# Kernel optimization log

Measured on AMD Instinct MI355X. Metric: run time of the kernel, lower is better.

Reference implementation:

```python
import jax, jax.numpy as jnp
import numpy as np

DEPTH = 10
N_FEATURES = 1024
N_INTERNAL = 2 ** DEPTH - 1  # 1023
N_LEAVES = 2 ** DEPTH        # 1024
BATCH = 16384


def setup_inputs() -> dict:
    key = jax.random.key(0)
    k_x, k_w, k_b, k_leaf = jax.random.split(key, 4)
    x = jax.random.normal(k_x, (BATCH, N_FEATURES), dtype=jnp.float32)
    # stacked nn.Linear(n_features, 1) weights for all internal nodes
    bound = 1.0 / np.sqrt(N_FEATURES)
    W = jax.random.uniform(k_w, (N_INTERNAL, N_FEATURES), dtype=jnp.float32, minval=-bound, maxval=bound)
    b = jax.random.uniform(k_b, (N_INTERNAL,), dtype=jnp.float32, minval=-bound, maxval=bound)
    leaf_values = jax.random.normal(k_leaf, (N_LEAVES, 1), dtype=jnp.float32) * 0.01
    return {"x": x, "W": W, "b": b, "leaf_values": leaf_values}


def reference(x, W, b, leaf_values):
    # all node gates in one GEMM: [B, n_internal]
    gates = jax.nn.sigmoid(x @ W.T + b)
    # leaf path bits, MSB-first (matches path[::-1] in the original).
    # NOTE: original code increments node_index 0..depth-1 for every leaf
    # (it does NOT do binary-tree child indexing) -- replicated faithfully.
    leaf_ids = jnp.arange(N_LEAVES)
    shifts = DEPTH - 1 - jnp.arange(DEPTH)
    bits = ((leaf_ids[:, None] >> shifts[None, :]) & 1).astype(bool)  # [L, D]
    prob = jnp.ones((x.shape[0], N_LEAVES), dtype=x.dtype)  # [B, L]
    for d in range(DEPTH):  # small fixed loop over tree depth
        p = gates[:, d:d + 1]  # [B, 1]
        prob = prob * jnp.where(bits[:, d][None, :], p, 1.0 - p)
    return prob @ leaf_values  # [B, 1]
```

## Files before the change

### kernel.cpp

```cpp
#include <hip/hip_runtime.h>

#define BATCH      16384
#define NF         1024
#define TREE_DEPTH 10

__global__ __launch_bounds__(256, 2)
void sdt_kernel(const float* __restrict__ x,
                const float* __restrict__ W,
                const float* __restrict__ b,
                const float* __restrict__ leaf,
                float* __restrict__ out,
                int nwaves_total)
{
    const int lane = threadIdx.x & 63;
    const int wid  = (int)((blockIdx.x * blockDim.x + threadIdx.x) >> 6);

    float4 Wr[10][4];
#pragma unroll
    for (int d = 0; d < 10; ++d)
#pragma unroll
        for (int k = 0; k < 4; ++k)
            Wr[d][k] = *reinterpret_cast<const float4*>(W + d * NF + k * 256 + 4 * lane);

    float bias[10];
#pragma unroll
    for (int d = 0; d < 10; ++d) bias[d] = b[d];

    float Lv[16];
#pragma unroll
    for (int k = 0; k < 4; ++k) {
        float4 t = *reinterpret_cast<const float4*>(leaf + 16 * lane + 4 * k);
        Lv[4 * k + 0] = t.x; Lv[4 * k + 1] = t.y;
        Lv[4 * k + 2] = t.z; Lv[4 * k + 3] = t.w;
    }

    float4 xv[4];
    {
        const float* xr = x + (size_t)wid * NF;
#pragma unroll
        for (int k = 0; k < 4; ++k)
            xv[k] = *reinterpret_cast<const float4*>(xr + k * 256 + 4 * lane);
    }

    for (int row = wid; row < BATCH; row += nwaves_total) {
        float4 xn[4];
        const int nrow = row + nwaves_total;
        if (nrow < BATCH) {
            const float* xr = x + (size_t)nrow * NF;
#pragma unroll
            for (int k = 0; k < 4; ++k)
                xn[k] = *reinterpret_cast<const float4*>(xr + k * 256 + 4 * lane);
        }

        float acc[10];
#pragma unroll
        for (int d = 0; d < 10; ++d) {
            float a = 0.0f;
#pragma unroll
            for (int k = 0; k < 4; ++k) {
                a = fmaf(xv[k].x, Wr[d][k].x, a);
                a = fmaf(xv[k].y, Wr[d][k].y, a);
                a = fmaf(xv[k].z, Wr[d][k].z, a);
                a = fmaf(xv[k].w, Wr[d][k].w, a);
            }
            acc[d] = a;
        }

#pragma unroll
        for (int d = 0; d < 10; ++d) {
            float a = acc[d];
#pragma unroll
            for (int off = 32; off > 0; off >>= 1)
                a += __shfl_xor(a, off, 64);
            acc[d] = a;
        }

        float g[10];
#pragma unroll
        for (int d = 0; d < 10; ++d) {
            float z = acc[d] + bias[d];
            g[d] = __builtin_amdgcn_rcpf(1.0f + __expf(-z));
        }

        float s9[8];
#pragma unroll
        for (int j = 0; j < 8; ++j)
            s9[j] = fmaf(g[9], Lv[2 * j + 1] - Lv[2 * j], Lv[2 * j]);
        float s8[4];
#pragma unroll
        for (int j = 0; j < 4; ++j)
            s8[j] = fmaf(g[8], s9[2 * j + 1] - s9[2 * j], s9[2 * j]);
        float s7[2];
#pragma unroll
        for (int j = 0; j < 2; ++j)
            s7[j] = fmaf(g[7], s8[2 * j + 1] - s8[2 * j], s8[2 * j]);
        float s6 = fmaf(g[6], s7[1] - s7[0], s7[0]);

        float w = 1.0f;
#pragma unroll
        for (int d = 0; d < 6; ++d) {
            int bit = (lane >> (5 - d)) & 1;
            w *= bit ? g[d] : (1.0f - g[d]);
        }

        float v = w * s6;
#pragma unroll
        for (int off = 32; off > 0; off >>= 1)
            v += __shfl_xor(v, off, 64);

        if (lane == 0) out[row] = v;

#pragma unroll
        for (int k = 0; k < 4; ++k) xv[k] = xn[k];
    }
}

extern "C" void kernel_launch(void* const* d_in, const int* in_sizes, int n_in,
                              void* d_out, int out_size, void* d_ws, size_t ws_size,
                              hipStream_t stream) {
    const float* x    = (const float*)d_in[0];
    const float* W    = (const float*)d_in[1];
    const float* b    = (const float*)d_in[2];
    const float* leaf = (const float*)d_in[3];
    float* out = (float*)d_out;

    const int blocks  = 512;
    const int threads = 256;
    const int nwaves  = blocks * threads / 64;

    sdt_kernel<<<blocks, threads, 0, stream>>>(x, W, b, leaf, out, nwaves);
}
```

Before: 26.25 us.

## Process two rows per wave iteration and move leaf values to LDS

Each wave now handles a pair of adjacent rows per loop iteration and prefetches the next pair, so twice as much x data is in flight. Leaf values are staged in shared memory and reloaded each iteration instead of staying resident in registers, which frees registers for the larger prefetch buffers. The larger working set raises register pressure and may hurt occupancy under the launch bounds. Batch and wave counts are now hard-coded constants.

```diff
diff --git a/kernel.cpp b/kernel.cpp
--- a/kernel.cpp
+++ b/kernel.cpp
@@ -1,19 +1,23 @@
 #include <hip/hip_runtime.h>
 
-#define BATCH      16384
-#define NF         1024
-#define TREE_DEPTH 10
+#define BATCH   16384
+#define NF      1024
+#define NWAVES  2048
+#define NPAIRS  (BATCH / 2 / NWAVES)
 
 __global__ __launch_bounds__(256, 2)
 void sdt_kernel(const float* __restrict__ x,
                 const float* __restrict__ W,
                 const float* __restrict__ b,
                 const float* __restrict__ leaf,
-                float* __restrict__ out,
-                int nwaves_total)
+                float* __restrict__ out)
 {
     const int lane = threadIdx.x & 63;
     const int wid  = (int)((blockIdx.x * blockDim.x + threadIdx.x) >> 6);
+
+    __shared__ float lv_s[1024];
+    *reinterpret_cast<float4*>(&lv_s[threadIdx.x * 4]) =
+        *reinterpret_cast<const float4*>(leaf + threadIdx.x * 4);
 
     float4 Wr[10][4];
 #pragma unroll
@@ -26,92 +30,131 @@
 #pragma unroll
     for (int d = 0; d < 10; ++d) bias[d] = b[d];
 
-    float Lv[16];
+    __syncthreads();
+
+    float4 xv[2][4];
+    {
+        const float* xr = x + (size_t)(2 * wid) * NF;
 #pragma unroll
-    for (int k = 0; k < 4; ++k) {
-        float4 t = *reinterpret_cast<const float4*>(leaf + 16 * lane + 4 * k);
-        Lv[4 * k + 0] = t.x; Lv[4 * k + 1] = t.y;
-        Lv[4 * k + 2] = t.z; Lv[4 * k + 3] = t.w;
+        for (int r = 0; r < 2; ++r)
+#pragma unroll
+            for (int k = 0; k < 4; ++k)
+                xv[r][k] = *reinterpret_cast<const float4*>(xr + r * NF + k * 256 + 4 * lane);
     }
 
-    float4 xv[4];
-    {
-        const float* xr = x + (size_t)wid * NF;
+    for (int i = 0; i < NPAIRS; ++i) {
+        const int rowA = 2 * (wid + i * NWAVES);
+
+        float4 xn[2][4];
+        if (i + 1 < NPAIRS) {
+            const float* xr = x + (size_t)(rowA + 2 * NWAVES) * NF;
 #pragma unroll
-        for (int k = 0; k < 4; ++k)
-            xv[k] = *reinterpret_cast<const float4*>(xr + k * 256 + 4 * lane);
-    }
-
-    for (int row = wid; row < BATCH; row += nwaves_total) {
-        float4 xn[4];
-        const int nrow = row + nwaves_total;
-        if (nrow < BATCH) {
-            const float* xr = x + (size_t)nrow * NF;
+            for (int r = 0; r < 2; ++r)
 #pragma unroll
-            for (int k = 0; k < 4; ++k)
-                xn[k] = *reinterpret_cast<const float4*>(xr + k * 256 + 4 * lane);
+                for (int k = 0; k < 4; ++k)
+                    xn[r][k] = *reinterpret_cast<const float4*>(xr + r * NF + k * 256 + 4 * lane);
         }
 
-        float acc[10];
+        float accA[10];
 #pragma unroll
         for (int d = 0; d < 10; ++d) {
             float a = 0.0f;
 #pragma unroll
             for (int k = 0; k < 4; ++k) {
-                a = fmaf(xv[k].x, Wr[d][k].x, a);
-                a = fmaf(xv[k].y, Wr[d][k].y, a);
-                a = fmaf(xv[k].z, Wr[d][k].z, a);
-                a = fmaf(xv[k].w, Wr[d][k].w, a);
+                a = fmaf(xv[0][k].x, Wr[d][k].x, a);
+                a = fmaf(xv[0][k].y, Wr[d][k].y, a);
+                a = fmaf(xv[0][k].z, Wr[d][k].z, a);
+                a = fmaf(xv[0][k].w, Wr[d][k].w, a);
             }
-            acc[d] = a;
+            accA[d] = a;
+        }
+#pragma unroll
+        for (int d = 0; d < 10; ++d) {
+            float a = accA[d];
+#pragma unroll
+            for (int off = 32; off > 0; off >>= 1)
+                a += __shfl_xor(a, off, 64);
+            accA[d] = a;
+        }
+
+        float accB[10];
+#pragma unroll
+        for (int d = 0; d < 10; ++d) {
+            float a = 0.0f;
+#pragma unroll
+            for (int k = 0; k < 4; ++k) {
+                a = fmaf(xv[1][k].x, Wr[d][k].x, a);
+                a = fmaf(xv[1][k].y, Wr[d][k].y, a);
+                a = fmaf(xv[1][k].z, Wr[d][k].z, a);
+                a = fmaf(xv[1][k].w, Wr[d][k].w, a);
+            }
+            accB[d] = a;
+        }
+#pragma unroll
+        for (int d = 0; d < 10; ++d) {
+            float a = accB[d];
+#pragma unroll
+            for (int off = 32; off > 0; off >>= 1)
+                a += __shfl_xor(a, off, 64);
+            accB[d] = a;
+        }
+
+        float g[2][10];
+#pragma unroll
+        for (int d = 0; d < 10; ++d) {
+            g[0][d] = __builtin_amdgcn_rcpf(1.0f + __expf(-(accA[d] + bias[d])));
+            g[1][d] = __builtin_amdgcn_rcpf(1.0f + __expf(-(accB[d] + bias[d])));
+        }
+
+        float Lv[16];
+#pragma unroll
+        for (int k = 0; k < 4; ++k) {
+            float4 t = *reinterpret_cast<const float4*>(&lv_s[16 * lane + 4 * k]);
+            Lv[4 * k + 0] = t.x; Lv[4 * k + 1] = t.y;
+            Lv[4 * k + 2] = t.z; Lv[4 * k + 3] = t.w;
+        }
+
+        float vout[2];
+#pragma unroll
+        for (int r = 0; r < 2; ++r) {
+            float s9[8];
+#pragma unroll
+            for (int j = 0; j < 8; ++j)
+                s9[j] = fmaf(g[r][9], Lv[2 * j + 1] - Lv[2 * j], Lv[2 * j]);
+            float s8[4];
+#pragma unroll
+            for (int j = 0; j < 4; ++j)
+                s8[j] = fmaf(g[r][8], s9[2 * j + 1] - s9[2 * j], s9[2 * j]);
+            float s7[2];
+#pragma unroll
+            for (int j = 0; j < 2; ++j)
+                s7[j] = fmaf(g[r][7], s8[2 * j + 1] - s8[2 * j], s8[2 * j]);
+            float s6 = fmaf(g[r][6], s7[1] - s7[0], s7[0]);
+
+            float w = 1.0f;
+#pragma unroll
+            for (int d = 0; d < 6; ++d) {
+                int bit = (lane >> (5 - d)) & 1;
+                w *= bit ? g[r][d] : (1.0f - g[r][d]);
+            }
+
+            float v = w * s6;
+#pragma unroll
+            for (int off = 32; off > 0; off >>= 1)
+                v += __shfl_xor(v, off, 64);
+            vout[r] = v;
+        }
+
+        if (lane == 0) {
+            out[rowA]     = vout[0];
+            out[rowA + 1] = vout[1];
         }
 
 #pragma unroll
-        for (int d = 0; d < 10; ++d) {
-            float a = acc[d];
+        for (int r = 0; r < 2; ++r)
 #pragma unroll
-            for (int off = 32; off > 0; off >>= 1)
-                a += __shfl_xor(a, off, 64);
-            acc[d] = a;
-        }
-
-        float g[10];
-#pragma unroll
-        for (int d = 0; d < 10; ++d) {
-            float z = acc[d] + bias[d];
-            g[d] = __builtin_amdgcn_rcpf(1.0f + __expf(-z));
-        }
-
-        float s9[8];
-#pragma unroll
-        for (int j = 0; j < 8; ++j)
-            s9[j] = fmaf(g[9], Lv[2 * j + 1] - Lv[2 * j], Lv[2 * j]);
-        float s8[4];
-#pragma unroll
-        for (int j = 0; j < 4; ++j)
-            s8[j] = fmaf(g[8], s9[2 * j + 1] - s9[2 * j], s9[2 * j]);
-        float s7[2];
-#pragma unroll
-        for (int j = 0; j < 2; ++j)
-            s7[j] = fmaf(g[7], s8[2 * j + 1] - s8[2 * j], s8[2 * j]);
-        float s6 = fmaf(g[6], s7[1] - s7[0], s7[0]);
-
-        float w = 1.0f;
-#pragma unroll
-        for (int d = 0; d < 6; ++d) {
-            int bit = (lane >> (5 - d)) & 1;
-            w *= bit ? g[d] : (1.0f - g[d]);
-        }
-
-        float v = w * s6;
-#pragma unroll
-        for (int off = 32; off > 0; off >>= 1)
-            v += __shfl_xor(v, off, 64);
-
-        if (lane == 0) out[row] = v;
-
-#pragma unroll
-        for (int k = 0; k < 4; ++k) xv[k] = xn[k];
+            for (int k = 0; k < 4; ++k)
+                xv[r][k] = xn[r][k];
     }
 }
 
@@ -126,7 +169,6 @@
 
     const int blocks  = 512;
     const int threads = 256;
-    const int nwaves  = blocks * threads / 64;
 
-    sdt_kernel<<<blocks, threads, 0, stream>>>(x, W, b, leaf, out, nwaves);
+    sdt_kernel<<<blocks, threads, 0, stream>>>(x, W, b, leaf, out);
 }
```

After: 29.88 us. 1.14x slower.
